# Kernel tuning notes

Measured on AMD Instinct MI355X. Metric: run time of the kernel, lower is better.

## Reference

```python
import jax, jax.numpy as jnp
import numpy as np
from jax import lax
import math

S, V, D, L, B = 64, 50257, 586, 4, 32  # seq_len, num_tokens, num_inputs, num_layers, batch_size
K1 = S // 4 + 1   # 17, conv1 kernel
P1 = S // 16 + 1  # 5,  avgpool1 kernel
P2 = S // 32 + 1  # 3,  avgpool2 kernel
EPS = 1e-5


def setup_inputs() -> dict:
    key = jax.random.key(0)
    ks = jax.random.split(key, 14)
    tokens = jax.random.randint(ks[0], (S, B), 0, V)
    emb = jax.random.normal(ks[1], (V, D - 3), jnp.float32) * 0.02
    # pos_embeds = randn(S,1,3).repeat(1,B,1)
    pos = jnp.tile(jax.random.normal(ks[2], (S, 1, 3), jnp.float32), (1, B, 1))
    gamma = 1.0 + 0.1 * jax.random.normal(ks[3], (L, S), jnp.float32)
    beta = 0.1 * jax.random.normal(ks[4], (L, S), jnp.float32)
    w1 = jax.random.normal(ks[5], (B // 2, B, K1), jnp.float32) * 0.02
    b1 = jax.random.normal(ks[6], (B // 2,), jnp.float32) * 0.02
    w2 = jax.random.normal(ks[7], (B // 4, B // 2, 1), jnp.float32) * 0.02
    b2 = jax.random.normal(ks[8], (B // 4,), jnp.float32) * 0.02
    w3 = jax.random.normal(ks[9], (B, B // 4, 3), jnp.float32) * 0.02
    b3 = jax.random.normal(ks[10], (B,), jnp.float32) * 0.02
    wl = jax.random.normal(ks[11], (128, 36), jnp.float32) * 0.1
    bl = jax.random.normal(ks[12], (128,), jnp.float32) * 0.1
    return {"tokens": tokens, "emb": emb, "pos": pos, "gamma": gamma, "beta": beta,
            "w1": w1, "b1": b1, "w2": w2, "b2": b2, "w3": w3, "b3": b3,
            "wl": wl, "bl": bl}


def _conv1d(x, w, b):
    # x: (N, C_in, Lx), w: (C_out, C_in, K)
    y = lax.conv_general_dilated(x, w, (1,), 'VALID',
                                 dimension_numbers=('NCH', 'OIH', 'NCH'))
    return y + b[None, :, None]


def _avgpool1d(x, k):
    # torch AvgPool1d: stride=kernel, floor mode
    n, c, lx = x.shape
    lo = lx // k
    return x[:, :, :lo * k].reshape(n, c, lo, k).mean(axis=-1)


def _logits(tokens, emb, pos, gamma, beta, w1, b1, w2, b2, w3, b3, wl, bl):
    x = emb[tokens] * math.sqrt(D)          # (S, B, D-3)
    x = jnp.concatenate([x, pos], axis=2)   # (S, B, D)
    for l in range(L):
        xb = x.swapaxes(0, 1)               # (B, S, D): BatchNorm1d over channels=S
        mean = xb.mean(axis=(0, 2), keepdims=True)
        var = xb.var(axis=(0, 2), keepdims=True)  # biased, training-mode batch stats
        xb = gamma[l][None, :, None] * (xb - mean) * lax.rsqrt(var + EPS) + beta[l][None, :, None]
        x = xb.swapaxes(0, 1)
    out = _conv1d(x, w1, b1)                # (S, B/2, D-16) = (64, 16, 570)
    out = _avgpool1d(out, P1)               # (64, 16, 114)
    out = _conv1d(out, w2, b2)              # (64, 8, 114)
    out = _avgpool1d(out, P2)               # (64, 8, 38)
    out = _conv1d(out, w3, b3)              # (64, 32, 36)
    out = jnp.einsum('sbk,vk->sbv', out, wl) + bl  # (64, 32, 128)
    return out


def reference(tokens, emb, pos, gamma, beta, w1, b1, w2, b2, w3, b3, wl, bl):
    out = _logits(tokens, emb, pos, gamma, beta, w1, b1, w2, b2, w3, b3, wl, bl)
    # vectorized replacement for the triple-nested .item() argmax loop
    return jnp.argmax(out, axis=-1).astype(jnp.float32)  # (S, B)
```

## Files before the change

kernel.cpp:

```cpp
#include <hip/hip_runtime.h>
#include <math.h>

#define SS 64
#define BB 32
#define DD 586
#define DE 583
#define U1 114
#define U2 38
#define T3 36
#define NTOK 18752
#define NSTAT (SS*BB)
#define WPN (32*21*16)
#define WPBLK (WPN/256)
#define SQD 24.207436873820409f


__global__ __launch_bounds__(256) void k_pre(
    const int* __restrict__ tokens, const float* __restrict__ emb,
    const float* __restrict__ pos, const float* __restrict__ w1,
    double* __restrict__ rowsumd, double* __restrict__ rowsqd,
    float* __restrict__ wp)
{
  const int bid = blockIdx.x, tid = threadIdx.x;
  if (bid < NSTAT) {
    const int s = bid >> 5, b = bid & 31;
    const int tok = tokens[s*BB + b];
    const float* row = emb + (size_t)tok*DE;
    double sum = 0.0, sq = 0.0;
    for (int d = tid; d < DE; d += 256) {
      float v = row[d] * SQD;
      sum += v; sq += (double)v*v;
    }
    if (tid < 3) {
      float v = pos[(s*BB + b)*3 + tid];
      sum += v; sq += (double)v*v;
    }
    for (int off = 32; off > 0; off >>= 1) {
      sum += __shfl_down(sum, off);
      sq  += __shfl_down(sq, off);
    }
    __shared__ double rs[4], rq[4];
    if ((tid & 63) == 0) { rs[tid>>6] = sum; rq[tid>>6] = sq; }
    __syncthreads();
    if (tid == 0) {
      rowsumd[bid] = (rs[0]+rs[1]) + (rs[2]+rs[3]);
      rowsqd[bid]  = (rq[0]+rq[1]) + (rq[2]+rq[3]);
    }
  } else {
    const int idx = (bid - NSTAT)*256 + tid;
    const int o = idx & 15;
    const int r = idx >> 4;
    const int m = r % 21;
    const int c = r / 21;
    int k0 = m - 4;  if (k0 < 0)  k0 = 0;
    int k1 = m;      if (k1 > 16) k1 = 16;
    float acc = 0.f;
    for (int k = k0; k <= k1; ++k) acc += w1[(o*BB + c)*17 + k];
    wp[idx] = acc * 0.2f;
  }
}

__global__ __launch_bounds__(256) void k_conv(
    const int* __restrict__ tokens, const float* __restrict__ emb,
    const float* __restrict__ pos, const float* __restrict__ wp,
    const double* __restrict__ rowsumd, const double* __restrict__ rowsqd,
    const float* __restrict__ gamma, const float* __restrict__ beta,
    float* __restrict__ part)
{
  const int s = blockIdx.x, g = blockIdx.y;
  const int tid = threadIdx.x;
  __shared__ float xs[8*DD];
  __shared__ int stok[8];
  __shared__ float sAl, sDe;
  if (tid < 8) stok[tid] = tokens[s*BB + g*8 + tid];
  __syncthreads();
  for (int i = tid; i < 8*DD; i += 256) {
    int cc = i / DD, d = i - cc*DD;
    float v = (d < DE) ? emb[(size_t)stok[cc]*DE + d] * SQD
                       : pos[(s*BB + g*8 + cc)*3 + (d - DE)];
    xs[i] = v;
  }
  if (tid < 32) {
    double sm = rowsumd[s*BB + tid], qq = rowsqd[s*BB + tid];
    for (int off = 16; off > 0; off >>= 1) {
      sm += __shfl_down(sm, off, 32);
      qq += __shfl_down(qq, off, 32);
    }
    if (tid == 0) {
      double m0d = sm / (double)NTOK;
      float m0 = (float)m0d;
      float v0 = (float)(qq / (double)NTOK - m0d*m0d);
      float a = 1.0f;
      for (int l = 0; l < 4; ++l) {
        float r = 1.0f / sqrtf(a*a*v0 + 1e-5f);
        a = gamma[l*SS + s] * r * a;
      }
      sAl = a;
      sDe = beta[3*SS + s] - a*m0;
    }
  }
  __syncthreads();
  const float al = sAl, de = sDe;
  const int up = tid & 127;
  const int oh = __builtin_amdgcn_readfirstlane(tid >> 7);
  const int u  = (up < U1) ? up : (U1 - 1);
  float acc[8] = {0,0,0,0,0,0,0,0};
  for (int cc = 0; cc < 8; ++cc) {
    const float* xr = &xs[cc*DD + 5*u];
    float xv[21];
    #pragma unroll
    for (int m = 0; m < 21; ++m) { float v = xr[m]; xv[m] = al * v + de; }
    const float* wr = wp + ((g*8 + cc)*21)*16 + oh*8;
    #pragma unroll
    for (int m = 0; m < 21; ++m) {
      #pragma unroll
      for (int j = 0; j < 8; ++j) acc[j] += xv[m] * wr[m*16 + j];
    }
  }
  if (up < U1) {
    float* pb = part + ((size_t)(g*SS + s)*16 + oh*8)*U1 + up;
    #pragma unroll
    for (int j = 0; j < 8; ++j) pb[j*U1] = acc[j];
  }
}

__global__ __launch_bounds__(256) void k_tail(
    const float* __restrict__ part, const float* __restrict__ b1,
    const float* __restrict__ w2, const float* __restrict__ b2,
    const float* __restrict__ w3, const float* __restrict__ b3,
    const float* __restrict__ wl, const float* __restrict__ bl,
    float* __restrict__ out)
{
  const int s = blockIdx.x, tid = threadIdx.x;
  __shared__ float o2[16*U1];
  __shared__ float p2[16*U2];
  __shared__ float o4[8*U2];
  __shared__ float o5[32*T3];
  __shared__ float wlb[128*37];
  __shared__ float blb[128];
  for (int idx = tid; idx < 128*36; idx += 256) {
    int v = idx / 36, t = idx - v*36;
    wlb[v*37 + t] = wl[idx];
  }
  if (tid < 128) blb[tid] = bl[tid];
  for (int idx = tid; idx < 16*U1; idx += 256) {
    int o = idx / U1;
    float acc = b1[o];
    acc += part[(size_t)(0*SS + s)*16*U1 + idx];
    acc += part[(size_t)(1*SS + s)*16*U1 + idx];
    acc += part[(size_t)(2*SS + s)*16*U1 + idx];
    acc += part[(size_t)(3*SS + s)*16*U1 + idx];
    o2[idx] = acc;
  }
  __syncthreads();
  for (int i2 = tid; i2 < 16*U2; i2 += 256) {
    int o = i2 / U2, v = i2 - o*U2;
    p2[i2] = (o2[o*U1 + 3*v] + o2[o*U1 + 3*v+1] + o2[o*U1 + 3*v+2]) * (1.f/3.f);
  }
  __syncthreads();
  for (int i2 = tid; i2 < 8*U2; i2 += 256) {
    int p = i2 / U2, v = i2 - p*U2;
    float acc = b2[p];
    #pragma unroll
    for (int o = 0; o < 16; ++o) acc += p2[o*U2 + v] * w2[p*16 + o];
    o4[i2] = acc;
  }
  __syncthreads();
  for (int i2 = tid; i2 < 32*T3; i2 += 256) {
    int q = i2 / T3, t = i2 - q*T3;
    float acc = b3[q];
    #pragma unroll
    for (int p = 0; p < 8; ++p) {
      acc += o4[p*U2 + t    ] * w3[(q*8+p)*3 + 0]
           + o4[p*U2 + t + 1] * w3[(q*8+p)*3 + 1]
           + o4[p*U2 + t + 2] * w3[(q*8+p)*3 + 2];
    }
    o5[i2] = acc;
  }
  __syncthreads();
  const int q = tid >> 3, vs = tid & 7;
  float best = -1e30f; int bidx = 0;
  const float* orow = &o5[q*T3];
  for (int i = 0; i < 16; ++i) {
    int v = vs + 8*i;
    float acc = blb[v];
    const float* wr = &wlb[v*37];
    #pragma unroll
    for (int t = 0; t < 36; ++t) acc += orow[t] * wr[t];
    if (acc > best) { best = acc; bidx = v; }
  }
  #pragma unroll
  for (int off = 1; off < 8; off <<= 1) {
    float ov = __shfl_xor(best, off);
    int oi = __shfl_xor(bidx, off);
    if (ov > best || (ov == best && oi < bidx)) { best = ov; bidx = oi; }
  }
  if (vs == 0) out[s*BB + q] = (float)bidx;
}

extern "C" void kernel_launch(void* const* d_in, const int* in_sizes, int n_in,
                              void* d_out, int out_size, void* d_ws, size_t ws_size,
                              hipStream_t stream)
{
  const int*   tokens = (const int*)  d_in[0];
  const float* emb    = (const float*)d_in[1];
  const float* pos    = (const float*)d_in[2];
  const float* gamma  = (const float*)d_in[3];
  const float* beta   = (const float*)d_in[4];
  const float* w1     = (const float*)d_in[5];
  const float* b1     = (const float*)d_in[6];
  const float* w2     = (const float*)d_in[7];
  const float* b2     = (const float*)d_in[8];
  const float* w3     = (const float*)d_in[9];
  const float* b3     = (const float*)d_in[10];
  const float* wl     = (const float*)d_in[11];
  const float* bl     = (const float*)d_in[12];
  float* out = (float*)d_out;

  double* rowsumd = (double*)d_ws;
  double* rowsqd  = rowsumd + NSTAT;
  float*  wp      = (float*)(rowsqd + NSTAT);
  float*  part    = wp + WPN;

  k_pre<<<dim3(NSTAT + WPBLK), dim3(256), 0, stream>>>(
      tokens, emb, pos, w1, rowsumd, rowsqd, wp);
  k_conv<<<dim3(SS, 4), dim3(256), 0, stream>>>(
      tokens, emb, pos, wp, rowsumd, rowsqd, gamma, beta, part);
  k_tail<<<dim3(SS), dim3(256), 0, stream>>>(part, b1, w2, b2, w3, b3,
                                             wl, bl, out);
}
```

Measured before the change: 201.6 us.

## Fuse stats into conv kernel and defer batchnorm affine to tail

Removes the separate stats/weight-prep kernel. The conv kernel now computes per-row sums while staging embeddings into shared memory, and convolves the raw (unnormalized) inputs. The batchnorm scale and shift are applied afterwards in the tail kernel through the linearity of the conv (al*conv + de*sum(w1)). This cuts one launch and one redundant gather of the embedding rows. In exchange, the conv inner loop reads w1 directly from global memory and computes a 5-tap box sum per channel, and rounding may differ slightly.

```diff
diff --git a/kernel.cpp b/kernel.cpp
--- a/kernel.cpp
+++ b/kernel.cpp
@@ -10,75 +10,103 @@
 #define T3 36
 #define NTOK 18752
 #define NSTAT (SS*BB)
-#define WPN (32*21*16)
-#define WPBLK (WPN/256)
 #define SQD 24.207436873820409f
 
 
-__global__ __launch_bounds__(256) void k_pre(
+__global__ __launch_bounds__(256) void k_main(
     const int* __restrict__ tokens, const float* __restrict__ emb,
     const float* __restrict__ pos, const float* __restrict__ w1,
     double* __restrict__ rowsumd, double* __restrict__ rowsqd,
-    float* __restrict__ wp)
-{
-  const int bid = blockIdx.x, tid = threadIdx.x;
-  if (bid < NSTAT) {
-    const int s = bid >> 5, b = bid & 31;
-    const int tok = tokens[s*BB + b];
-    const float* row = emb + (size_t)tok*DE;
-    double sum = 0.0, sq = 0.0;
-    for (int d = tid; d < DE; d += 256) {
-      float v = row[d] * SQD;
-      sum += v; sq += (double)v*v;
-    }
-    if (tid < 3) {
-      float v = pos[(s*BB + b)*3 + tid];
-      sum += v; sq += (double)v*v;
-    }
-    for (int off = 32; off > 0; off >>= 1) {
-      sum += __shfl_down(sum, off);
-      sq  += __shfl_down(sq, off);
-    }
-    __shared__ double rs[4], rq[4];
-    if ((tid & 63) == 0) { rs[tid>>6] = sum; rq[tid>>6] = sq; }
-    __syncthreads();
-    if (tid == 0) {
-      rowsumd[bid] = (rs[0]+rs[1]) + (rs[2]+rs[3]);
-      rowsqd[bid]  = (rq[0]+rq[1]) + (rq[2]+rq[3]);
-    }
-  } else {
-    const int idx = (bid - NSTAT)*256 + tid;
-    const int o = idx & 15;
-    const int r = idx >> 4;
-    const int m = r % 21;
-    const int c = r / 21;
-    int k0 = m - 4;  if (k0 < 0)  k0 = 0;
-    int k1 = m;      if (k1 > 16) k1 = 16;
-    float acc = 0.f;
-    for (int k = k0; k <= k1; ++k) acc += w1[(o*BB + c)*17 + k];
-    wp[idx] = acc * 0.2f;
-  }
-}
-
-__global__ __launch_bounds__(256) void k_conv(
-    const int* __restrict__ tokens, const float* __restrict__ emb,
-    const float* __restrict__ pos, const float* __restrict__ wp,
-    const double* __restrict__ rowsumd, const double* __restrict__ rowsqd,
-    const float* __restrict__ gamma, const float* __restrict__ beta,
     float* __restrict__ part)
 {
   const int s = blockIdx.x, g = blockIdx.y;
   const int tid = threadIdx.x;
   __shared__ float xs[8*DD];
   __shared__ int stok[8];
+  if (tid < 8) stok[tid] = tokens[s*BB + g*8 + tid];
+  __syncthreads();
+  {
+    const int rr = tid >> 5, l = tid & 31;
+    const float* row = emb + (size_t)stok[rr]*DE;
+    double sum = 0.0, sq = 0.0;
+    #pragma unroll
+    for (int j = 0; j < 19; ++j) {
+      int d = l + 32*j;
+      if (d < DD) {
+        float v = (d < DE) ? row[d] * SQD
+                           : pos[(s*BB + g*8 + rr)*3 + (d - DE)];
+        xs[rr*DD + d] = v;
+        sum += v; sq += (double)v*v;
+      }
+    }
+    for (int off = 16; off > 0; off >>= 1) {
+      sum += __shfl_down(sum, off, 32);
+      sq  += __shfl_down(sq, off, 32);
+    }
+    if (l == 0) {
+      rowsumd[s*BB + g*8 + rr] = sum;
+      rowsqd [s*BB + g*8 + rr] = sq;
+    }
+  }
+  __syncthreads();
+  const int up = tid & 127;
+  const int oh = __builtin_amdgcn_readfirstlane(tid >> 7);
+  const int u  = (up < U1) ? up : (U1 - 1);
+  float acc[8] = {0,0,0,0,0,0,0,0};
+  for (int cc = 0; cc < 8; ++cc) {
+    const float* xr = &xs[cc*DD + 5*u];
+    float xv[21];
+    #pragma unroll
+    for (int m = 0; m < 21; ++m) xv[m] = xr[m];
+    float xw[17];
+    #pragma unroll
+    for (int k = 0; k < 17; ++k)
+      xw[k] = ((xv[k] + xv[k+1]) + (xv[k+2] + xv[k+3])) + xv[k+4];
+    #pragma unroll
+    for (int j = 0; j < 8; ++j) {
+      const float* wj = w1 + ((size_t)(oh*8 + j)*BB + (g*8 + cc))*17;
+      float a = 0.f;
+      #pragma unroll
+      for (int k = 0; k < 17; ++k) a += xw[k] * wj[k];
+      acc[j] += a;
+    }
+  }
+  if (up < U1) {
+    float* pb = part + ((size_t)(g*SS + s)*16 + oh*8)*U1 + up;
+    #pragma unroll
+    for (int j = 0; j < 8; ++j) pb[j*U1] = acc[j] * 0.2f;
+  }
+}
+
+__global__ __launch_bounds__(256) void k_tail(
+    const double* __restrict__ rowsumd, const double* __restrict__ rowsqd,
+    const float* __restrict__ gamma, const float* __restrict__ beta,
+    const float* __restrict__ part, const float* __restrict__ w1,
+    const float* __restrict__ b1, const float* __restrict__ w2,
+    const float* __restrict__ b2, const float* __restrict__ w3,
+    const float* __restrict__ b3, const float* __restrict__ wl,
+    const float* __restrict__ bl, float* __restrict__ out)
+{
+  const int s = blockIdx.x, tid = threadIdx.x;
+  __shared__ float o2[16*U1];
+  __shared__ float p2[16*U2];
+  __shared__ float o4[8*U2];
+  __shared__ float o5[32*T3];
+  __shared__ float wlb[128*37];
+  __shared__ float blb[128];
+  __shared__ float wsumb[16];
   __shared__ float sAl, sDe;
-  if (tid < 8) stok[tid] = tokens[s*BB + g*8 + tid];
-  __syncthreads();
-  for (int i = tid; i < 8*DD; i += 256) {
-    int cc = i / DD, d = i - cc*DD;
-    float v = (d < DE) ? emb[(size_t)stok[cc]*DE + d] * SQD
-                       : pos[(s*BB + g*8 + cc)*3 + (d - DE)];
-    xs[i] = v;
+  for (int idx = tid; idx < 128*36; idx += 256) {
+    int v = idx / 36, t = idx - v*36;
+    wlb[v*37 + t] = wl[idx];
+  }
+  if (tid < 128) blb[tid] = bl[tid];
+  {
+    const int o = tid >> 4, i = tid & 15;
+    float acc = 0.f;
+    for (int j = i; j < BB*17; j += 16) acc += w1[o*BB*17 + j];
+    for (int off = 8; off > 0; off >>= 1) acc += __shfl_down(acc, off, 16);
+    if (i == 0) wsumb[o] = acc;
   }
   if (tid < 32) {
     double sm = rowsumd[s*BB + tid], qq = rowsqd[s*BB + tid];
@@ -101,56 +129,13 @@
   }
   __syncthreads();
   const float al = sAl, de = sDe;
-  const int up = tid & 127;
-  const int oh = __builtin_amdgcn_readfirstlane(tid >> 7);
-  const int u  = (up < U1) ? up : (U1 - 1);
-  float acc[8] = {0,0,0,0,0,0,0,0};
-  for (int cc = 0; cc < 8; ++cc) {
-    const float* xr = &xs[cc*DD + 5*u];
-    float xv[21];
-    #pragma unroll
-    for (int m = 0; m < 21; ++m) { float v = xr[m]; xv[m] = al * v + de; }
-    const float* wr = wp + ((g*8 + cc)*21)*16 + oh*8;
-    #pragma unroll
-    for (int m = 0; m < 21; ++m) {
-      #pragma unroll
-      for (int j = 0; j < 8; ++j) acc[j] += xv[m] * wr[m*16 + j];
-    }
-  }
-  if (up < U1) {
-    float* pb = part + ((size_t)(g*SS + s)*16 + oh*8)*U1 + up;
-    #pragma unroll
-    for (int j = 0; j < 8; ++j) pb[j*U1] = acc[j];
-  }
-}
-
-__global__ __launch_bounds__(256) void k_tail(
-    const float* __restrict__ part, const float* __restrict__ b1,
-    const float* __restrict__ w2, const float* __restrict__ b2,
-    const float* __restrict__ w3, const float* __restrict__ b3,
-    const float* __restrict__ wl, const float* __restrict__ bl,
-    float* __restrict__ out)
-{
-  const int s = blockIdx.x, tid = threadIdx.x;
-  __shared__ float o2[16*U1];
-  __shared__ float p2[16*U2];
-  __shared__ float o4[8*U2];
-  __shared__ float o5[32*T3];
-  __shared__ float wlb[128*37];
-  __shared__ float blb[128];
-  for (int idx = tid; idx < 128*36; idx += 256) {
-    int v = idx / 36, t = idx - v*36;
-    wlb[v*37 + t] = wl[idx];
-  }
-  if (tid < 128) blb[tid] = bl[tid];
   for (int idx = tid; idx < 16*U1; idx += 256) {
     int o = idx / U1;
-    float acc = b1[o];
-    acc += part[(size_t)(0*SS + s)*16*U1 + idx];
-    acc += part[(size_t)(1*SS + s)*16*U1 + idx];
-    acc += part[(size_t)(2*SS + s)*16*U1 + idx];
-    acc += part[(size_t)(3*SS + s)*16*U1 + idx];
-    o2[idx] = acc;
+    float psum = part[(size_t)(0*SS + s)*16*U1 + idx]
+               + part[(size_t)(1*SS + s)*16*U1 + idx]
+               + part[(size_t)(2*SS + s)*16*U1 + idx]
+               + part[(size_t)(3*SS + s)*16*U1 + idx];
+    o2[idx] = al*psum + de*wsumb[o] + b1[o];
   }
   __syncthreads();
   for (int i2 = tid; i2 < 16*U2; i2 += 256) {
@@ -219,13 +204,11 @@
 
   double* rowsumd = (double*)d_ws;
   double* rowsqd  = rowsumd + NSTAT;
-  float*  wp      = (float*)(rowsqd + NSTAT);
-  float*  part    = wp + WPN;
-
-  k_pre<<<dim3(NSTAT + WPBLK), dim3(256), 0, stream>>>(
-      tokens, emb, pos, w1, rowsumd, rowsqd, wp);
-  k_conv<<<dim3(SS, 4), dim3(256), 0, stream>>>(
-      tokens, emb, pos, wp, rowsumd, rowsqd, gamma, beta, part);
-  k_tail<<<dim3(SS), dim3(256), 0, stream>>>(part, b1, w2, b2, w3, b3,
-                                             wl, bl, out);
+  float*  part    = (float*)(rowsqd + NSTAT);
+
+  k_main<<<dim3(SS, 4), dim3(256), 0, stream>>>(
+      tokens, emb, pos, w1, rowsumd, rowsqd, part);
+  k_tail<<<dim3(SS), dim3(256), 0, stream>>>(
+      rowsumd, rowsqd, gamma, beta, part, w1, b1, w2, b2, w3, b3,
+      wl, bl, out);
 }
```

After: 193.5 us. 4.0% less time.
